# Kernel tuning notes

Measured on AMD Instinct MI355X. Metric: run time of the kernel, lower is better.

The kernel has to match this reference:

```python
import jax, jax.numpy as jnp
import numpy as np

B, S, H, D, R = 2, 2048, 16, 128, 16
HID = H * D
ROPE_BASE = 10000.0


def _rotate_half(x):
    x1, x2 = x[..., : D // 2], x[..., D // 2:]
    return jnp.concatenate((-x2, x1), axis=-1)


def _sin_cos(position_ids):
    # full-dim RoPE (rope_fraction == 1)
    inv_freq = 1.0 / (ROPE_BASE ** (jnp.arange(0, D, 2, dtype=jnp.float32) / D))  # [D/2]
    freqs = position_ids.astype(jnp.float32)[..., None] * inv_freq  # [B,S,D/2]
    emb = jnp.concatenate((freqs, freqs), axis=-1)  # [B,S,D]
    # add head axis -> [B,1,S,D]
    return jnp.sin(emb)[:, None], jnp.cos(emb)[:, None]


def setup_inputs() -> dict:
    key = jax.random.key(0)
    ks = jax.random.split(key, 6)
    q = jax.random.normal(ks[0], (B, S, HID), dtype=jnp.float32)
    k = jax.random.normal(ks[1], (B, S, HID), dtype=jnp.float32)
    v = jax.random.normal(ks[2], (B, S, HID), dtype=jnp.float32)
    position_ids = jnp.tile(jnp.arange(S, dtype=jnp.int64)[None], (B, 1))
    causal = jnp.tril(jnp.ones((S, S), dtype=bool))
    attention_mask = jnp.where(causal, 0.0, -1e9).astype(jnp.float32)
    attention_mask = jnp.broadcast_to(attention_mask[None, None], (B, 1, S, S))
    k_registers = jax.random.normal(ks[3], (1, H, R, D), dtype=jnp.float32)
    v_registers = jax.random.normal(ks[4], (1, H, R, D), dtype=jnp.float32)
    return {
        "query_states": q,
        "key_states": k,
        "value_states": v,
        "position_ids": position_ids,
        "attention_mask": attention_mask,
        "k_registers": k_registers,
        "v_registers": v_registers,
    }


def reference(query_states, key_states, value_states, position_ids,
              attention_mask, k_registers, v_registers):
    bsz, q_len, _ = query_states.shape
    # [B,S,H*D] -> [B,H,S,D]
    q = query_states.reshape(bsz, q_len, H, D).transpose(0, 2, 1, 3)
    k = key_states.reshape(bsz, -1, H, D).transpose(0, 2, 1, 3)
    v = value_states.reshape(bsz, -1, H, D).transpose(0, 2, 1, 3)

    sin, cos = _sin_cos(position_ids)
    q = q * cos + _rotate_half(q) * sin
    k = k * cos + _rotate_half(k) * sin

    # concat learned register K/V tokens along kv-length
    k = jnp.concatenate((k, jnp.broadcast_to(k_registers, (bsz, H, R, D))), axis=2)
    v = jnp.concatenate((v, jnp.broadcast_to(v_registers, (bsz, H, R, D))), axis=2)
    mask = jnp.concatenate(
        (attention_mask,
         jnp.zeros(attention_mask.shape[:-1] + (R,), dtype=attention_mask.dtype)),
        axis=-1)

    scale = 1.0 / np.sqrt(D).astype(np.float32)
    scores = jnp.einsum('bhqd,bhkd->bhqk', q, k * scale) + mask  # [B,H,S,S+R]
    probs = jax.nn.softmax(scores.astype(jnp.float32), axis=-1).astype(q.dtype)
    out = jnp.einsum('bhqk,bhkd->bhqd', probs, v)
    return out.transpose(0, 2, 1, 3).reshape(bsz, q_len, H * D)
```

## Files before the change

kernel.cpp:

```cpp
#include <hip/hip_runtime.h>

#define S_LEN 2048
#define HID   2048
#define NH    16
#define HD    128
#define NREG  16
#define KPAD  2112
#define NBH   32

typedef float f32x4 __attribute__((ext_vector_type(4)));
typedef short s16x8 __attribute__((ext_vector_type(8)));

__device__ __forceinline__ unsigned short f2bf(float f) {
    union { float f; unsigned int u; } x; x.f = f;
    return (unsigned short)((x.u + 0x7FFFu + ((x.u >> 16) & 1u)) >> 16);
}
__device__ __forceinline__ unsigned short f2bf_t(float f) {
    union { float f; unsigned int u; } x; x.f = f;
    return (unsigned short)(x.u >> 16);
}
__device__ __forceinline__ void gl_lds16(const unsigned short* g, unsigned short* l) {
    __builtin_amdgcn_global_load_lds((const __attribute__((address_space(1))) void*)g,
                                     (__attribute__((address_space(3))) void*)l, 16, 0, 0);
}

__global__ void rope_qk_kernel(const float* __restrict__ q, const float* __restrict__ k,
                               const int* __restrict__ pos,
                               unsigned short* __restrict__ Qb, unsigned short* __restrict__ Kb) {
    int i = blockIdx.x * 256 + threadIdx.x;
    int dh = i & 63;
    int h  = (i >> 6) & 15;
    int s  = (i >> 10) & 2047;
    int b  = i >> 21;
    float p   = (float)pos[b * S_LEN + s];
    float inv = exp2f((float)dh * -0.20762050593046014f);
    float ang = p * inv;
    float rev = ang * 0.15915494309189535f;
    rev -= rintf(rev);
    float a2 = rev * 6.283185307179586f;
    float sn = __sinf(a2), cs = __cosf(a2);
    const float* qp = q + (size_t)(b * S_LEN + s) * HID + h * HD + dh;
    const float* kp = k + (size_t)(b * S_LEN + s) * HID + h * HD + dh;
    float q1 = qp[0], q2 = qp[64];
    float k1 = kp[0], k2 = kp[64];
    const float scale = 0.08838834764831845f;
    size_t qo = (size_t)((b * NH + h) * S_LEN + s) * HD + dh;
    Qb[qo]      = f2bf((q1 * cs - q2 * sn) * scale);
    Qb[qo + 64] = f2bf((q2 * cs + q1 * sn) * scale);
    size_t ko = (size_t)((b * NH + h) * KPAD + s) * HD + dh;
    Kb[ko]      = f2bf(k1 * cs - k2 * sn);
    Kb[ko + 64] = f2bf(k2 * cs + k1 * sn);
}

__global__ void fill_regs_kernel(const float* __restrict__ kreg, const float* __restrict__ vreg,
                                 unsigned short* __restrict__ Kb, unsigned short* __restrict__ Vt) {
    int i = blockIdx.x * 256 + threadIdx.x;
    {
        int d = i & 127, r = (i >> 7) & 63, h = (i >> 13) & 15, b = i >> 17;
        float v = (r < NREG) ? kreg[(h * NREG + r) * HD + d] : 0.0f;
        Kb[((size_t)((b * NH + h) * KPAD + 2048 + r)) * HD + d] = f2bf(v);
    }
    {
        int r = i & 63, d = (i >> 6) & 127, h = (i >> 13) & 15, b = i >> 17;
        float v = (r < NREG) ? vreg[(h * NREG + r) * HD + d] : 0.0f;
        Vt[((size_t)((b * NH + h) * HD + d)) * KPAD + 2048 + r] = f2bf(v);
    }
}

__global__ void transpose_v_kernel(const float* __restrict__ v, unsigned short* __restrict__ Vt) {
    __shared__ unsigned short T[64][136];
    int t  = threadIdx.x;
    int bh = blockIdx.x >> 5, st = blockIdx.x & 31;
    int b  = bh >> 4, h = bh & 15;
    {
        int key = t >> 2, c = t & 3;
        const float* src = v + (size_t)(b * S_LEN + st * 64 + key) * HID + h * HD;
        #pragma unroll
        for (int i = 0; i < 4; ++i) {
            int d0 = c * 32 + i * 8;
            float4 a  = *(const float4*)(src + d0);
            float4 bb = *(const float4*)(src + d0 + 4);
            unsigned short tmp[8] = { f2bf(a.x), f2bf(a.y), f2bf(a.z), f2bf(a.w),
                                      f2bf(bb.x), f2bf(bb.y), f2bf(bb.z), f2bf(bb.w) };
            *(uint4*)(&T[key][d0]) = *(const uint4*)tmp;
        }
    }
    __syncthreads();
    {
        int d = t >> 1, half = t & 1;
        unsigned short buf[32];
        #pragma unroll
        for (int i = 0; i < 32; ++i) buf[i] = T[half * 32 + i][d];
        uint4* dst = (uint4*)(Vt + ((size_t)(bh * HD + d)) * KPAD + st * 64 + half * 32);
        const uint4* bp = (const uint4*)buf;
        #pragma unroll
        for (int i = 0; i < 4; ++i) dst[i] = bp[i];
    }
}

__global__ __launch_bounds__(256, 2)
void attn_kernel(const unsigned short* __restrict__ Qb, const unsigned short* __restrict__ Kb,
                 const unsigned short* __restrict__ Vt, float* __restrict__ out) {
    __shared__ unsigned short Klds[64 * 128];
    __shared__ unsigned short Vtl[128 * 64];
    __shared__ unsigned short Plds[4 * 32 * 72];

    int idx = blockIdx.x;
    int bh  = idx & 31;
    int j5  = idx >> 5;
    int t   = (idx < 256) ? (15 - 2 * j5) : (2 * (j5 - 8));
    int b = bh >> 4, h = bh & 15;
    int tid = threadIdx.x, w = tid >> 6, lane = tid & 63;
    int quad = lane >> 4, k15 = lane & 15;
    int s0q = t * 128;

    const unsigned short* kg[4]; unsigned short* klp[4];
    const unsigned short* vg[4]; unsigned short* vlp[4];
    {
        int krow = 16 * w + (lane >> 4);
        #pragma unroll
        for (int j = 0; j < 4; ++j) {
            int key = krow + 4 * j;
            kg[j]  = Kb + ((size_t)bh * KPAD + key) * HD + (((lane & 15) ^ (key & 15)) << 3);
            klp[j] = Klds + (16 * w + 4 * j) * HD;
        }
        int drow = 32 * w + (lane >> 3);
        int vsw  = ((lane & 7) ^ (lane >> 3)) << 3;
        #pragma unroll
        for (int j = 0; j < 4; ++j) {
            vg[j]  = Vt + ((size_t)bh * HD + drow + 8 * j) * KPAD + vsw;
            vlp[j] = Vtl + (32 * w + 8 * j) * 64;
        }
    }

    s16x8 qa[2][4];
    #pragma unroll
    for (int mt = 0; mt < 2; ++mt) {
        const unsigned short* qrow =
            Qb + ((size_t)bh * S_LEN + s0q + w * 32 + mt * 16 + k15) * HD + quad * 8;
        #pragma unroll
        for (int kc = 0; kc < 4; ++kc) qa[mt][kc] = *(const s16x8*)(qrow + kc * 32);
    }

    f32x4 oacc[2][8];
    float lsum[2][4];
    #pragma unroll
    for (int mt = 0; mt < 2; ++mt) {
        #pragma unroll
        for (int nc = 0; nc < 8; ++nc) oacc[mt][nc] = (f32x4){0.f, 0.f, 0.f, 0.f};
        #pragma unroll
        for (int r = 0; r < 4; ++r) lsum[mt][r] = 0.f;
    }

    auto stage = [&](int kbase) {
        size_t ko = (size_t)kbase * HD;
        #pragma unroll
        for (int j = 0; j < 4; ++j) gl_lds16(kg[j] + ko, klp[j]);
        #pragma unroll
        for (int j = 0; j < 4; ++j) gl_lds16(vg[j] + kbase, vlp[j]);
    };

    auto tile = [&](int coff, int mode) {
        #pragma unroll
        for (int mt = 0; mt < 2; ++mt) {
            f32x4 sc[4] = {};
            #pragma unroll
            for (int nc = 0; nc < 4; ++nc) {
                if (mode == 2 && nc > 0) continue;
                #pragma unroll
                for (int kc = 0; kc < 4; ++kc) {
                    const s16x8 bf = *(const s16x8*)(Klds + (nc * 16 + k15) * HD +
                                                     (((4 * kc + quad) ^ k15) << 3));
                    sc[nc] = __builtin_amdgcn_mfma_f32_16x16x32_bf16(qa[mt][kc], bf, sc[nc], 0, 0, 0);
                }
            }
            int rowb = w * 32 + mt * 16 + quad * 4;
            #pragma unroll
            for (int r = 0; r < 4; ++r) {
                float p[4];
                #pragma unroll
                for (int nc = 0; nc < 4; ++nc) {
                    if (mode == 2 && nc > 0) { p[nc] = 0.f; continue; }
                    float e = __expf(sc[nc][r]);
                    bool valid = (mode != 1) || (coff + nc * 16 + k15 <= rowb + r);
                    p[nc] = valid ? e : 0.f;
                }
                lsum[mt][r] += (p[0] + p[1]) + (p[2] + p[3]);
                int prow = w * (32 * 72) + (mt * 16 + quad * 4 + r) * 72 + k15;
                Plds[prow]      = f2bf_t(p[0]);
                Plds[prow + 16] = f2bf_t(p[1]);
                Plds[prow + 32] = f2bf_t(p[2]);
                Plds[prow + 48] = f2bf_t(p[3]);
            }
        }
        #pragma unroll
        for (int mt = 0; mt < 2; ++mt)
            #pragma unroll
            for (int kc = 0; kc < 2; ++kc) {
                const s16x8 pf = *(const s16x8*)(Plds + w * (32 * 72) +
                                                 (mt * 16 + k15) * 72 + kc * 32 + quad * 8);
                #pragma unroll
                for (int nc = 0; nc < 8; ++nc) {
                    const s16x8 vf = *(const s16x8*)(Vtl + (nc * 16 + k15) * 64 +
                                                     (((4 * kc + quad) ^ (k15 & 7)) << 3));
                    oacc[mt][nc] = __builtin_amdgcn_mfma_f32_16x16x32_bf16(pf, vf, oacc[mt][nc], 0, 0, 0);
                }
            }
    };

    int nfull = 2 * t;
    for (int kt = 0; kt < nfull; ++kt) {
        __syncthreads();
        stage(kt * 64);
        __syncthreads();
        tile(0, 0);
    }
    #pragma unroll
    for (int dt = 0; dt < 2; ++dt) {
        __syncthreads();
        stage((2 * t + dt) * 64);
        __syncthreads();
        tile(64 * dt, 1);
    }
    __syncthreads();
    stage(2048);
    __syncthreads();
    tile(0, 2);

    #pragma unroll
    for (int mt = 0; mt < 2; ++mt)
        #pragma unroll
        for (int r = 0; r < 4; ++r) {
            float lv = lsum[mt][r];
            #pragma unroll
            for (int off = 1; off < 16; off <<= 1) lv += __shfl_xor(lv, off);
            float invl = 1.0f / lv;
            size_t row = (size_t)(b * S_LEN + s0q + w * 32 + mt * 16 + quad * 4 + r) * HID
                         + h * HD + k15;
            #pragma unroll
            for (int nc = 0; nc < 8; ++nc)
                out[row + nc * 16] = oacc[mt][nc][r] * invl;
        }
}

extern "C" void kernel_launch(void* const* d_in, const int* in_sizes, int n_in,
                              void* d_out, int out_size, void* d_ws, size_t ws_size,
                              hipStream_t stream) {
    const float* q    = (const float*)d_in[0];
    const float* k    = (const float*)d_in[1];
    const float* v    = (const float*)d_in[2];
    const int*   pos  = (const int*)d_in[3];
    const float* kreg = (const float*)d_in[5];
    const float* vreg = (const float*)d_in[6];
    float* out = (float*)d_out;

    unsigned short* Qb = (unsigned short*)d_ws;
    unsigned short* Kb = Qb + (size_t)NBH * S_LEN * HD;
    unsigned short* Vt = Kb + (size_t)NBH * KPAD * HD;

    rope_qk_kernel<<<dim3(16384), dim3(256), 0, stream>>>(q, k, pos, Qb, Kb);
    fill_regs_kernel<<<dim3(1024), dim3(256), 0, stream>>>(kreg, vreg, Kb, Vt);
    transpose_v_kernel<<<dim3(1024), dim3(256), 0, stream>>>(v, Vt);
    attn_kernel<<<dim3(512), dim3(256), 0, stream>>>(Qb, Kb, Vt, out);
}
```

Baseline: 224.0 us.

## Merge prepass kernels and restructure attention with double-buffered V and paired tiles

The three preprocessing kernels (RoPE, register fill, V transpose) are merged into one launch, and the RoPE path is vectorized to four elements per thread. The attention kernel moves to 512 threads with 16 query rows per wave. Each block processes a pair of causal tiles (t and 15-t) so work is balanced. V is double-buffered and the next tile's loads are issued before softmax, using manual vmcnt waits, s_barrier and setprio to overlap loads with MFMA. Fewer launches and better latency hiding are traded for more complex synchronization, and the hand-written waitcnt counts could be fragile.

```diff
diff --git a/kernel.cpp b/kernel.cpp
--- a/kernel.cpp
+++ b/kernel.cpp
@@ -23,224 +23,247 @@
     __builtin_amdgcn_global_load_lds((const __attribute__((address_space(1))) void*)g,
                                      (__attribute__((address_space(3))) void*)l, 16, 0, 0);
 }
-
-__global__ void rope_qk_kernel(const float* __restrict__ q, const float* __restrict__ k,
-                               const int* __restrict__ pos,
-                               unsigned short* __restrict__ Qb, unsigned short* __restrict__ Kb) {
-    int i = blockIdx.x * 256 + threadIdx.x;
-    int dh = i & 63;
-    int h  = (i >> 6) & 15;
-    int s  = (i >> 10) & 2047;
-    int b  = i >> 21;
-    float p   = (float)pos[b * S_LEN + s];
-    float inv = exp2f((float)dh * -0.20762050593046014f);
-    float ang = p * inv;
-    float rev = ang * 0.15915494309189535f;
-    rev -= rintf(rev);
-    float a2 = rev * 6.283185307179586f;
-    float sn = __sinf(a2), cs = __cosf(a2);
-    const float* qp = q + (size_t)(b * S_LEN + s) * HID + h * HD + dh;
-    const float* kp = k + (size_t)(b * S_LEN + s) * HID + h * HD + dh;
-    float q1 = qp[0], q2 = qp[64];
-    float k1 = kp[0], k2 = kp[64];
-    const float scale = 0.08838834764831845f;
-    size_t qo = (size_t)((b * NH + h) * S_LEN + s) * HD + dh;
-    Qb[qo]      = f2bf((q1 * cs - q2 * sn) * scale);
-    Qb[qo + 64] = f2bf((q2 * cs + q1 * sn) * scale);
-    size_t ko = (size_t)((b * NH + h) * KPAD + s) * HD + dh;
-    Kb[ko]      = f2bf(k1 * cs - k2 * sn);
-    Kb[ko + 64] = f2bf(k2 * cs + k1 * sn);
-}
-
-__global__ void fill_regs_kernel(const float* __restrict__ kreg, const float* __restrict__ vreg,
-                                 unsigned short* __restrict__ Kb, unsigned short* __restrict__ Vt) {
-    int i = blockIdx.x * 256 + threadIdx.x;
-    {
-        int d = i & 127, r = (i >> 7) & 63, h = (i >> 13) & 15, b = i >> 17;
-        float v = (r < NREG) ? kreg[(h * NREG + r) * HD + d] : 0.0f;
-        Kb[((size_t)((b * NH + h) * KPAD + 2048 + r)) * HD + d] = f2bf(v);
+#define VMWAIT(n) asm volatile("s_waitcnt vmcnt(" #n ")" ::: "memory")
+__device__ __forceinline__ void bar() { asm volatile("s_barrier" ::: "memory"); }
+
+__global__ void prepass_kernel(const float* __restrict__ q, const float* __restrict__ k,
+                               const float* __restrict__ v, const int* __restrict__ pos,
+                               const float* __restrict__ kreg, const float* __restrict__ vreg,
+                               unsigned short* __restrict__ Qb, unsigned short* __restrict__ Kb,
+                               unsigned short* __restrict__ Vt) {
+    __shared__ unsigned short T[64][136];
+    int bid = blockIdx.x, tid = threadIdx.x;
+
+    if (bid < 4096) {
+        int i  = bid * 256 + tid;
+        int d4 = (i & 15) << 2;
+        int h  = (i >> 4) & 15;
+        int s  = (i >> 8) & 2047;
+        int b  = i >> 19;
+        float p = (float)pos[b * S_LEN + s];
+        const float* qp = q + (size_t)(b * S_LEN + s) * HID + h * HD + d4;
+        const float* kp = k + (size_t)(b * S_LEN + s) * HID + h * HD + d4;
+        float4 q1 = *(const float4*)qp, q2 = *(const float4*)(qp + 64);
+        float4 k1 = *(const float4*)kp, k2 = *(const float4*)(kp + 64);
+        const float* q1f = (const float*)&q1; const float* q2f = (const float*)&q2;
+        const float* k1f = (const float*)&k1; const float* k2f = (const float*)&k2;
+        const float scale = 0.08838834764831845f;
+        unsigned short oq1[4], oq2[4], ok1[4], ok2[4];
+        #pragma unroll
+        for (int j = 0; j < 4; ++j) {
+            float inv = exp2f((float)(d4 + j) * -0.20762050593046014f);
+            float rev = p * inv * 0.15915494309189535f;
+            rev -= rintf(rev);
+            float a2 = rev * 6.283185307179586f;
+            float sn = __sinf(a2), cs = __cosf(a2);
+            oq1[j] = f2bf((q1f[j] * cs - q2f[j] * sn) * scale);
+            oq2[j] = f2bf((q2f[j] * cs + q1f[j] * sn) * scale);
+            ok1[j] = f2bf(k1f[j] * cs - k2f[j] * sn);
+            ok2[j] = f2bf(k2f[j] * cs + k1f[j] * sn);
+        }
+        uint2 a;
+        size_t qo = (size_t)((b * NH + h) * S_LEN + s) * HD + d4;
+        a.x = (unsigned)oq1[0] | ((unsigned)oq1[1] << 16);
+        a.y = (unsigned)oq1[2] | ((unsigned)oq1[3] << 16);
+        *(uint2*)(Qb + qo) = a;
+        a.x = (unsigned)oq2[0] | ((unsigned)oq2[1] << 16);
+        a.y = (unsigned)oq2[2] | ((unsigned)oq2[3] << 16);
+        *(uint2*)(Qb + qo + 64) = a;
+        size_t ko = (size_t)((b * NH + h) * KPAD + s) * HD + d4;
+        a.x = (unsigned)ok1[0] | ((unsigned)ok1[1] << 16);
+        a.y = (unsigned)ok1[2] | ((unsigned)ok1[3] << 16);
+        *(uint2*)(Kb + ko) = a;
+        a.x = (unsigned)ok2[0] | ((unsigned)ok2[1] << 16);
+        a.y = (unsigned)ok2[2] | ((unsigned)ok2[3] << 16);
+        *(uint2*)(Kb + ko + 64) = a;
+    } else if (bid < 5120) {
+        int vb = bid - 4096;
+        int tt = tid;
+        int bh = vb >> 5, st = vb & 31;
+        int b  = bh >> 4, h = bh & 15;
+        {
+            int key = tt >> 2, c = tt & 3;
+            const float* src = v + (size_t)(b * S_LEN + st * 64 + key) * HID + h * HD;
+            #pragma unroll
+            for (int i = 0; i < 4; ++i) {
+                int d0 = c * 32 + i * 8;
+                float4 aa = *(const float4*)(src + d0);
+                float4 bb = *(const float4*)(src + d0 + 4);
+                unsigned short tmp[8] = { f2bf(aa.x), f2bf(aa.y), f2bf(aa.z), f2bf(aa.w),
+                                          f2bf(bb.x), f2bf(bb.y), f2bf(bb.z), f2bf(bb.w) };
+                *(uint4*)(&T[key][d0]) = *(const uint4*)tmp;
+            }
+        }
+        __syncthreads();
+        {
+            int d = tt >> 1, half = tt & 1;
+            unsigned short buf[32];
+            #pragma unroll
+            for (int i = 0; i < 32; ++i) buf[i] = T[half * 32 + i][d];
+            uint4* dst = (uint4*)(Vt + ((size_t)(bh * HD + d)) * KPAD + st * 64 + half * 32);
+            const uint4* bp = (const uint4*)buf;
+            #pragma unroll
+            for (int i = 0; i < 4; ++i) dst[i] = bp[i];
+        }
+    } else {
+        int i = (bid - 5120) * 256 + tid;
+        {
+            int d = i & 127, r = (i >> 7) & 63, h = (i >> 13) & 15, b = i >> 17;
+            float x = (r < NREG) ? kreg[(h * NREG + r) * HD + d] : 0.0f;
+            Kb[((size_t)((b * NH + h) * KPAD + 2048 + r)) * HD + d] = f2bf(x);
+        }
+        {
+            int r = i & 63, d = (i >> 6) & 127, h = (i >> 13) & 15, b = i >> 17;
+            float x = (r < NREG) ? vreg[(h * NREG + r) * HD + d] : 0.0f;
+            Vt[((size_t)((b * NH + h) * HD + d)) * KPAD + 2048 + r] = f2bf(x);
+        }
     }
-    {
-        int r = i & 63, d = (i >> 6) & 127, h = (i >> 13) & 15, b = i >> 17;
-        float v = (r < NREG) ? vreg[(h * NREG + r) * HD + d] : 0.0f;
-        Vt[((size_t)((b * NH + h) * HD + d)) * KPAD + 2048 + r] = f2bf(v);
-    }
-}
-
-__global__ void transpose_v_kernel(const float* __restrict__ v, unsigned short* __restrict__ Vt) {
-    __shared__ unsigned short T[64][136];
-    int t  = threadIdx.x;
-    int bh = blockIdx.x >> 5, st = blockIdx.x & 31;
-    int b  = bh >> 4, h = bh & 15;
-    {
-        int key = t >> 2, c = t & 3;
-        const float* src = v + (size_t)(b * S_LEN + st * 64 + key) * HID + h * HD;
-        #pragma unroll
-        for (int i = 0; i < 4; ++i) {
-            int d0 = c * 32 + i * 8;
-            float4 a  = *(const float4*)(src + d0);
-            float4 bb = *(const float4*)(src + d0 + 4);
-            unsigned short tmp[8] = { f2bf(a.x), f2bf(a.y), f2bf(a.z), f2bf(a.w),
-                                      f2bf(bb.x), f2bf(bb.y), f2bf(bb.z), f2bf(bb.w) };
-            *(uint4*)(&T[key][d0]) = *(const uint4*)tmp;
-        }
-    }
-    __syncthreads();
-    {
-        int d = t >> 1, half = t & 1;
-        unsigned short buf[32];
-        #pragma unroll
-        for (int i = 0; i < 32; ++i) buf[i] = T[half * 32 + i][d];
-        uint4* dst = (uint4*)(Vt + ((size_t)(bh * HD + d)) * KPAD + st * 64 + half * 32);
-        const uint4* bp = (const uint4*)buf;
-        #pragma unroll
-        for (int i = 0; i < 4; ++i) dst[i] = bp[i];
-    }
-}
-
-__global__ __launch_bounds__(256, 2)
+}
+
+__global__ __launch_bounds__(512, 2)
 void attn_kernel(const unsigned short* __restrict__ Qb, const unsigned short* __restrict__ Kb,
                  const unsigned short* __restrict__ Vt, float* __restrict__ out) {
     __shared__ unsigned short Klds[64 * 128];
-    __shared__ unsigned short Vtl[128 * 64];
-    __shared__ unsigned short Plds[4 * 32 * 72];
+    __shared__ unsigned short Vtl[2 * 128 * 64];
+    __shared__ unsigned short Plds[8 * 16 * 72];
 
     int idx = blockIdx.x;
     int bh  = idx & 31;
-    int j5  = idx >> 5;
-    int t   = (idx < 256) ? (15 - 2 * j5) : (2 * (j5 - 8));
+    int pr  = idx >> 5;
     int b = bh >> 4, h = bh & 15;
     int tid = threadIdx.x, w = tid >> 6, lane = tid & 63;
     int quad = lane >> 4, k15 = lane & 15;
-    int s0q = t * 128;
-
-    const unsigned short* kg[4]; unsigned short* klp[4];
-    const unsigned short* vg[4]; unsigned short* vlp[4];
-    {
-        int krow = 16 * w + (lane >> 4);
-        #pragma unroll
-        for (int j = 0; j < 4; ++j) {
-            int key = krow + 4 * j;
-            kg[j]  = Kb + ((size_t)bh * KPAD + key) * HD + (((lane & 15) ^ (key & 15)) << 3);
-            klp[j] = Klds + (16 * w + 4 * j) * HD;
-        }
-        int drow = 32 * w + (lane >> 3);
-        int vsw  = ((lane & 7) ^ (lane >> 3)) << 3;
-        #pragma unroll
-        for (int j = 0; j < 4; ++j) {
-            vg[j]  = Vt + ((size_t)bh * HD + drow + 8 * j) * KPAD + vsw;
-            vlp[j] = Vtl + (32 * w + 8 * j) * 64;
-        }
+
+    const unsigned short* kgb[2]; unsigned short* klp[2];
+    const unsigned short* vgb[2]; int vlo[2];
+    #pragma unroll
+    for (int j = 0; j < 2; ++j) {
+        int krow = 8 * w + 4 * j + (lane >> 4);
+        kgb[j] = Kb + ((size_t)bh * KPAD + krow) * HD + (((lane & 15) ^ (krow & 15)) << 3);
+        klp[j] = Klds + (8 * w + 4 * j) * HD;
+        int vrow = 16 * w + 8 * j + (lane >> 3);
+        vgb[j] = Vt + ((size_t)bh * HD + vrow) * KPAD + (((lane & 7) ^ ((lane >> 3) & 7)) << 3);
+        vlo[j] = (16 * w + 8 * j) * 64;
     }
-
-    s16x8 qa[2][4];
-    #pragma unroll
-    for (int mt = 0; mt < 2; ++mt) {
-        const unsigned short* qrow =
-            Qb + ((size_t)bh * S_LEN + s0q + w * 32 + mt * 16 + k15) * HD + quad * 8;
-        #pragma unroll
-        for (int kc = 0; kc < 4; ++kc) qa[mt][kc] = *(const s16x8*)(qrow + kc * 32);
-    }
-
-    f32x4 oacc[2][8];
-    float lsum[2][4];
-    #pragma unroll
-    for (int mt = 0; mt < 2; ++mt) {
-        #pragma unroll
-        for (int nc = 0; nc < 8; ++nc) oacc[mt][nc] = (f32x4){0.f, 0.f, 0.f, 0.f};
-        #pragma unroll
-        for (int r = 0; r < 4; ++r) lsum[mt][r] = 0.f;
-    }
-
-    auto stage = [&](int kbase) {
+    auto stageK = [&](int kbase) {
         size_t ko = (size_t)kbase * HD;
-        #pragma unroll
-        for (int j = 0; j < 4; ++j) gl_lds16(kg[j] + ko, klp[j]);
-        #pragma unroll
-        for (int j = 0; j < 4; ++j) gl_lds16(vg[j] + kbase, vlp[j]);
+        gl_lds16(kgb[0] + ko, klp[0]);
+        gl_lds16(kgb[1] + ko, klp[1]);
     };
-
-    auto tile = [&](int coff, int mode) {
-        #pragma unroll
-        for (int mt = 0; mt < 2; ++mt) {
+    auto stageV = [&](int kbase, int buf) {
+        unsigned short* vbuf = Vtl + buf * (128 * 64);
+        gl_lds16(vgb[0] + kbase, vbuf + vlo[0]);
+        gl_lds16(vgb[1] + kbase, vbuf + vlo[1]);
+    };
+
+    #pragma unroll 1
+    for (int half = 0; half < 2; ++half) {
+        int t   = half ? (15 - pr) : pr;
+        int s0q = t * 128;
+        int NT  = 2 * t + 3;
+
+        s16x8 qa[4];
+        {
+            const unsigned short* qrow =
+                Qb + ((size_t)bh * S_LEN + s0q + w * 16 + k15) * HD + quad * 8;
+            #pragma unroll
+            for (int kc = 0; kc < 4; ++kc) qa[kc] = *(const s16x8*)(qrow + kc * 32);
+        }
+        f32x4 oacc[8];
+        float lsum[4];
+        #pragma unroll
+        for (int nc = 0; nc < 8; ++nc) oacc[nc] = (f32x4){0.f, 0.f, 0.f, 0.f};
+        #pragma unroll
+        for (int r = 0; r < 4; ++r) lsum[r] = 0.f;
+
+        stageK(0);
+        stageV(0, 0);
+        VMWAIT(2);
+        bar();
+
+        int cur = 0;
+        #pragma unroll 1
+        for (int kt = 0; kt < NT; ++kt) {
+            int  mode = (kt < 2 * t) ? 0 : ((kt < 2 * t + 2) ? 1 : 2);
+            int  coff = 64 * (kt - 2 * t);
+            bool more = (kt + 1 < NT);
+            int  nkb  = (kt + 1 < 2 * t + 2) ? (kt + 1) * 64 : 2048;
+
             f32x4 sc[4] = {};
+            __builtin_amdgcn_s_setprio(1);
             #pragma unroll
             for (int nc = 0; nc < 4; ++nc) {
-                if (mode == 2 && nc > 0) continue;
-                #pragma unroll
-                for (int kc = 0; kc < 4; ++kc) {
-                    const s16x8 bf = *(const s16x8*)(Klds + (nc * 16 + k15) * HD +
-                                                     (((4 * kc + quad) ^ k15) << 3));
-                    sc[nc] = __builtin_amdgcn_mfma_f32_16x16x32_bf16(qa[mt][kc], bf, sc[nc], 0, 0, 0);
+                if (!(mode == 2 && nc > 0)) {
+                    #pragma unroll
+                    for (int kc = 0; kc < 4; ++kc) {
+                        const s16x8 bf = *(const s16x8*)(Klds + (nc * 16 + k15) * HD +
+                                                         (((4 * kc + quad) ^ k15) << 3));
+                        sc[nc] = __builtin_amdgcn_mfma_f32_16x16x32_bf16(qa[kc], bf, sc[nc], 0, 0, 0);
+                    }
                 }
             }
-            int rowb = w * 32 + mt * 16 + quad * 4;
+            __builtin_amdgcn_s_setprio(0);
+            bar();
+
+            if (more) { stageK(nkb); stageV(nkb, cur ^ 1); }
+
+            int rowb = w * 16 + quad * 4;
             #pragma unroll
             for (int r = 0; r < 4; ++r) {
-                float p[4];
+                float pv[4];
                 #pragma unroll
                 for (int nc = 0; nc < 4; ++nc) {
-                    if (mode == 2 && nc > 0) { p[nc] = 0.f; continue; }
+                    if (mode == 2 && nc > 0) { pv[nc] = 0.f; continue; }
                     float e = __expf(sc[nc][r]);
                     bool valid = (mode != 1) || (coff + nc * 16 + k15 <= rowb + r);
-                    p[nc] = valid ? e : 0.f;
+                    pv[nc] = valid ? e : 0.f;
                 }
-                lsum[mt][r] += (p[0] + p[1]) + (p[2] + p[3]);
-                int prow = w * (32 * 72) + (mt * 16 + quad * 4 + r) * 72 + k15;
-                Plds[prow]      = f2bf_t(p[0]);
-                Plds[prow + 16] = f2bf_t(p[1]);
-                Plds[prow + 32] = f2bf_t(p[2]);
-                Plds[prow + 48] = f2bf_t(p[3]);
-            }
-        }
-        #pragma unroll
-        for (int mt = 0; mt < 2; ++mt)
+                lsum[r] += (pv[0] + pv[1]) + (pv[2] + pv[3]);
+                int prow = w * 1152 + (quad * 4 + r) * 72 + k15;
+                Plds[prow]      = f2bf_t(pv[0]);
+                Plds[prow + 16] = f2bf_t(pv[1]);
+                Plds[prow + 32] = f2bf_t(pv[2]);
+                Plds[prow + 48] = f2bf_t(pv[3]);
+            }
+
+            if (more) { VMWAIT(4); } else { VMWAIT(0); }
+            bar();
+
+            const unsigned short* Vc = Vtl + cur * (128 * 64);
+            __builtin_amdgcn_s_setprio(1);
             #pragma unroll
             for (int kc = 0; kc < 2; ++kc) {
-                const s16x8 pf = *(const s16x8*)(Plds + w * (32 * 72) +
-                                                 (mt * 16 + k15) * 72 + kc * 32 + quad * 8);
-                #pragma unroll
-                for (int nc = 0; nc < 8; ++nc) {
-                    const s16x8 vf = *(const s16x8*)(Vtl + (nc * 16 + k15) * 64 +
-                                                     (((4 * kc + quad) ^ (k15 & 7)) << 3));
-                    oacc[mt][nc] = __builtin_amdgcn_mfma_f32_16x16x32_bf16(pf, vf, oacc[mt][nc], 0, 0, 0);
+                if (!(mode == 2 && kc > 0)) {
+                    const s16x8 pf = *(const s16x8*)(Plds + w * 1152 + k15 * 72 +
+                                                     kc * 32 + quad * 8);
+                    #pragma unroll
+                    for (int nc = 0; nc < 8; ++nc) {
+                        const s16x8 vf = *(const s16x8*)(Vc + (nc * 16 + k15) * 64 +
+                                                         (((4 * kc + quad) ^ (k15 & 7)) << 3));
+                        oacc[nc] = __builtin_amdgcn_mfma_f32_16x16x32_bf16(pf, vf, oacc[nc], 0, 0, 0);
+                    }
                 }
             }
-    };
-
-    int nfull = 2 * t;
-    for (int kt = 0; kt < nfull; ++kt) {
-        __syncthreads();
-        stage(kt * 64);
-        __syncthreads();
-        tile(0, 0);
-    }
-    #pragma unroll
-    for (int dt = 0; dt < 2; ++dt) {
-        __syncthreads();
-        stage((2 * t + dt) * 64);
-        __syncthreads();
-        tile(64 * dt, 1);
-    }
-    __syncthreads();
-    stage(2048);
-    __syncthreads();
-    tile(0, 2);
-
-    #pragma unroll
-    for (int mt = 0; mt < 2; ++mt)
+            __builtin_amdgcn_s_setprio(0);
+
+            if (more) { VMWAIT(2); }
+            bar();
+            cur ^= 1;
+        }
+
         #pragma unroll
         for (int r = 0; r < 4; ++r) {
-            float lv = lsum[mt][r];
+            float lv = lsum[r];
             #pragma unroll
             for (int off = 1; off < 16; off <<= 1) lv += __shfl_xor(lv, off);
             float invl = 1.0f / lv;
-            size_t row = (size_t)(b * S_LEN + s0q + w * 32 + mt * 16 + quad * 4 + r) * HID
+            size_t row = (size_t)(b * S_LEN + s0q + w * 16 + quad * 4 + r) * HID
                          + h * HD + k15;
             #pragma unroll
             for (int nc = 0; nc < 8; ++nc)
-                out[row + nc * 16] = oacc[mt][nc][r] * invl;
-        }
+                out[row + nc * 16] = oacc[nc][r] * invl;
+        }
+    }
 }
 
 extern "C" void kernel_launch(void* const* d_in, const int* in_sizes, int n_in,
@@ -258,8 +281,6 @@
     unsigned short* Kb = Qb + (size_t)NBH * S_LEN * HD;
     unsigned short* Vt = Kb + (size_t)NBH * KPAD * HD;
 
-    rope_qk_kernel<<<dim3(16384), dim3(256), 0, stream>>>(q, k, pos, Qb, Kb);
-    fill_regs_kernel<<<dim3(1024), dim3(256), 0, stream>>>(kreg, vreg, Kb, Vt);
-    transpose_v_kernel<<<dim3(1024), dim3(256), 0, stream>>>(v, Vt);
-    attn_kernel<<<dim3(512), dim3(256), 0, stream>>>(Qb, Kb, Vt, out);
-}
+    prepass_kernel<<<dim3(6144), dim3(256), 0, stream>>>(q, k, v, pos, kreg, vreg, Qb, Kb, Vt);
+    attn_kernel<<<dim3(256), dim3(512), 0, stream>>>(Qb, Kb, Vt, out);
+}
```

Measured after the change: 231.6 us. 3.4% more time.

## Merge prepass kernels into one launch and reorder MFMA loops for fragment reuse

Applied to the files above, without the earlier changes.

Folds the RoPE, V-transpose and register-fill kernels into a single prepass launch split by block index. The RoPE part now handles four elements per thread with float4 loads and packed stores. In the attention tile, the m-tile loop is moved inside so each K and V LDS fragment feeds two MFMAs, and the MFMA sections are wrapped in s_setprio. The PV stage also skips the unused kc chunk in the register-tile mode. These aim to cut launch overhead and LDS reads, but the larger live score array raises register pressure.

```diff
diff --git a/kernel.cpp b/kernel.cpp
--- a/kernel.cpp
+++ b/kernel.cpp
@@ -24,77 +24,97 @@
                                      (__attribute__((address_space(3))) void*)l, 16, 0, 0);
 }
 
-__global__ void rope_qk_kernel(const float* __restrict__ q, const float* __restrict__ k,
-                               const int* __restrict__ pos,
-                               unsigned short* __restrict__ Qb, unsigned short* __restrict__ Kb) {
-    int i = blockIdx.x * 256 + threadIdx.x;
-    int dh = i & 63;
-    int h  = (i >> 6) & 15;
-    int s  = (i >> 10) & 2047;
-    int b  = i >> 21;
-    float p   = (float)pos[b * S_LEN + s];
-    float inv = exp2f((float)dh * -0.20762050593046014f);
-    float ang = p * inv;
-    float rev = ang * 0.15915494309189535f;
-    rev -= rintf(rev);
-    float a2 = rev * 6.283185307179586f;
-    float sn = __sinf(a2), cs = __cosf(a2);
-    const float* qp = q + (size_t)(b * S_LEN + s) * HID + h * HD + dh;
-    const float* kp = k + (size_t)(b * S_LEN + s) * HID + h * HD + dh;
-    float q1 = qp[0], q2 = qp[64];
-    float k1 = kp[0], k2 = kp[64];
-    const float scale = 0.08838834764831845f;
-    size_t qo = (size_t)((b * NH + h) * S_LEN + s) * HD + dh;
-    Qb[qo]      = f2bf((q1 * cs - q2 * sn) * scale);
-    Qb[qo + 64] = f2bf((q2 * cs + q1 * sn) * scale);
-    size_t ko = (size_t)((b * NH + h) * KPAD + s) * HD + dh;
-    Kb[ko]      = f2bf(k1 * cs - k2 * sn);
-    Kb[ko + 64] = f2bf(k2 * cs + k1 * sn);
-}
-
-__global__ void fill_regs_kernel(const float* __restrict__ kreg, const float* __restrict__ vreg,
-                                 unsigned short* __restrict__ Kb, unsigned short* __restrict__ Vt) {
-    int i = blockIdx.x * 256 + threadIdx.x;
-    {
-        int d = i & 127, r = (i >> 7) & 63, h = (i >> 13) & 15, b = i >> 17;
-        float v = (r < NREG) ? kreg[(h * NREG + r) * HD + d] : 0.0f;
-        Kb[((size_t)((b * NH + h) * KPAD + 2048 + r)) * HD + d] = f2bf(v);
-    }
-    {
-        int r = i & 63, d = (i >> 6) & 127, h = (i >> 13) & 15, b = i >> 17;
-        float v = (r < NREG) ? vreg[(h * NREG + r) * HD + d] : 0.0f;
-        Vt[((size_t)((b * NH + h) * HD + d)) * KPAD + 2048 + r] = f2bf(v);
-    }
-}
-
-__global__ void transpose_v_kernel(const float* __restrict__ v, unsigned short* __restrict__ Vt) {
+__global__ void prepass_kernel(const float* __restrict__ q, const float* __restrict__ k,
+                               const float* __restrict__ v, const int* __restrict__ pos,
+                               const float* __restrict__ kreg, const float* __restrict__ vreg,
+                               unsigned short* __restrict__ Qb, unsigned short* __restrict__ Kb,
+                               unsigned short* __restrict__ Vt) {
     __shared__ unsigned short T[64][136];
-    int t  = threadIdx.x;
-    int bh = blockIdx.x >> 5, st = blockIdx.x & 31;
-    int b  = bh >> 4, h = bh & 15;
-    {
-        int key = t >> 2, c = t & 3;
-        const float* src = v + (size_t)(b * S_LEN + st * 64 + key) * HID + h * HD;
-        #pragma unroll
-        for (int i = 0; i < 4; ++i) {
-            int d0 = c * 32 + i * 8;
-            float4 a  = *(const float4*)(src + d0);
-            float4 bb = *(const float4*)(src + d0 + 4);
-            unsigned short tmp[8] = { f2bf(a.x), f2bf(a.y), f2bf(a.z), f2bf(a.w),
-                                      f2bf(bb.x), f2bf(bb.y), f2bf(bb.z), f2bf(bb.w) };
-            *(uint4*)(&T[key][d0]) = *(const uint4*)tmp;
-        }
-    }
-    __syncthreads();
-    {
-        int d = t >> 1, half = t & 1;
-        unsigned short buf[32];
-        #pragma unroll
-        for (int i = 0; i < 32; ++i) buf[i] = T[half * 32 + i][d];
-        uint4* dst = (uint4*)(Vt + ((size_t)(bh * HD + d)) * KPAD + st * 64 + half * 32);
-        const uint4* bp = (const uint4*)buf;
-        #pragma unroll
-        for (int i = 0; i < 4; ++i) dst[i] = bp[i];
+    int bid = blockIdx.x, tid = threadIdx.x;
+
+    if (bid < 4096) {
+        int i  = bid * 256 + tid;
+        int d4 = (i & 15) << 2;
+        int h  = (i >> 4) & 15;
+        int s  = (i >> 8) & 2047;
+        int b  = i >> 19;
+        float p = (float)pos[b * S_LEN + s];
+        const float* qp = q + (size_t)(b * S_LEN + s) * HID + h * HD + d4;
+        const float* kp = k + (size_t)(b * S_LEN + s) * HID + h * HD + d4;
+        float4 q1 = *(const float4*)qp, q2 = *(const float4*)(qp + 64);
+        float4 k1 = *(const float4*)kp, k2 = *(const float4*)(kp + 64);
+        const float* q1f = (const float*)&q1; const float* q2f = (const float*)&q2;
+        const float* k1f = (const float*)&k1; const float* k2f = (const float*)&k2;
+        const float scale = 0.08838834764831845f;
+        unsigned short oq1[4], oq2[4], ok1[4], ok2[4];
+        #pragma unroll
+        for (int j = 0; j < 4; ++j) {
+            float inv = exp2f((float)(d4 + j) * -0.20762050593046014f);
+            float rev = p * inv * 0.15915494309189535f;
+            rev -= rintf(rev);
+            float a2 = rev * 6.283185307179586f;
+            float sn = __sinf(a2), cs = __cosf(a2);
+            oq1[j] = f2bf((q1f[j] * cs - q2f[j] * sn) * scale);
+            oq2[j] = f2bf((q2f[j] * cs + q1f[j] * sn) * scale);
+            ok1[j] = f2bf(k1f[j] * cs - k2f[j] * sn);
+            ok2[j] = f2bf(k2f[j] * cs + k1f[j] * sn);
+        }
+        uint2 a;
+        size_t qo = (size_t)((b * NH + h) * S_LEN + s) * HD + d4;
+        a.x = (unsigned)oq1[0] | ((unsigned)oq1[1] << 16);
+        a.y = (unsigned)oq1[2] | ((unsigned)oq1[3] << 16);
+        *(uint2*)(Qb + qo) = a;
+        a.x = (unsigned)oq2[0] | ((unsigned)oq2[1] << 16);
+        a.y = (unsigned)oq2[2] | ((unsigned)oq2[3] << 16);
+        *(uint2*)(Qb + qo + 64) = a;
+        size_t ko = (size_t)((b * NH + h) * KPAD + s) * HD + d4;
+        a.x = (unsigned)ok1[0] | ((unsigned)ok1[1] << 16);
+        a.y = (unsigned)ok1[2] | ((unsigned)ok1[3] << 16);
+        *(uint2*)(Kb + ko) = a;
+        a.x = (unsigned)ok2[0] | ((unsigned)ok2[1] << 16);
+        a.y = (unsigned)ok2[2] | ((unsigned)ok2[3] << 16);
+        *(uint2*)(Kb + ko + 64) = a;
+    } else if (bid < 5120) {
+        int vb = bid - 4096;
+        int tt = tid;
+        int bh = vb >> 5, st = vb & 31;
+        int b  = bh >> 4, h = bh & 15;
+        {
+            int key = tt >> 2, c = tt & 3;
+            const float* src = v + (size_t)(b * S_LEN + st * 64 + key) * HID + h * HD;
+            #pragma unroll
+            for (int i = 0; i < 4; ++i) {
+                int d0 = c * 32 + i * 8;
+                float4 aa = *(const float4*)(src + d0);
+                float4 bb = *(const float4*)(src + d0 + 4);
+                unsigned short tmp[8] = { f2bf(aa.x), f2bf(aa.y), f2bf(aa.z), f2bf(aa.w),
+                                          f2bf(bb.x), f2bf(bb.y), f2bf(bb.z), f2bf(bb.w) };
+                *(uint4*)(&T[key][d0]) = *(const uint4*)tmp;
+            }
+        }
+        __syncthreads();
+        {
+            int d = tt >> 1, half = tt & 1;
+            unsigned short buf[32];
+            #pragma unroll
+            for (int i = 0; i < 32; ++i) buf[i] = T[half * 32 + i][d];
+            uint4* dst = (uint4*)(Vt + ((size_t)(bh * HD + d)) * KPAD + st * 64 + half * 32);
+            const uint4* bp = (const uint4*)buf;
+            #pragma unroll
+            for (int i = 0; i < 4; ++i) dst[i] = bp[i];
+        }
+    } else {
+        int i = (bid - 5120) * 256 + tid;
+        {
+            int d = i & 127, r = (i >> 7) & 63, h = (i >> 13) & 15, b = i >> 17;
+            float x = (r < NREG) ? kreg[(h * NREG + r) * HD + d] : 0.0f;
+            Kb[((size_t)((b * NH + h) * KPAD + 2048 + r)) * HD + d] = f2bf(x);
+        }
+        {
+            int r = i & 63, d = (i >> 6) & 127, h = (i >> 13) & 15, b = i >> 17;
+            float x = (r < NREG) ? vreg[(h * NREG + r) * HD + d] : 0.0f;
+            Vt[((size_t)((b * NH + h) * HD + d)) * KPAD + 2048 + r] = f2bf(x);
+        }
     }
 }
 
@@ -161,19 +181,26 @@
     };
 
     auto tile = [&](int coff, int mode) {
-        #pragma unroll
-        for (int mt = 0; mt < 2; ++mt) {
-            f32x4 sc[4] = {};
-            #pragma unroll
-            for (int nc = 0; nc < 4; ++nc) {
-                if (mode == 2 && nc > 0) continue;
+        f32x4 sc[2][4] = {};
+        __builtin_amdgcn_s_setprio(1);
+        #pragma unroll
+        for (int nc = 0; nc < 4; ++nc) {
+            if (!(mode == 2 && nc > 0)) {
                 #pragma unroll
                 for (int kc = 0; kc < 4; ++kc) {
                     const s16x8 bf = *(const s16x8*)(Klds + (nc * 16 + k15) * HD +
                                                      (((4 * kc + quad) ^ k15) << 3));
-                    sc[nc] = __builtin_amdgcn_mfma_f32_16x16x32_bf16(qa[mt][kc], bf, sc[nc], 0, 0, 0);
+                    #pragma unroll
+                    for (int mt = 0; mt < 2; ++mt)
+                        sc[mt][nc] = __builtin_amdgcn_mfma_f32_16x16x32_bf16(qa[mt][kc], bf,
+                                                                             sc[mt][nc], 0, 0, 0);
                 }
             }
+        }
+        __builtin_amdgcn_s_setprio(0);
+
+        #pragma unroll
+        for (int mt = 0; mt < 2; ++mt) {
             int rowb = w * 32 + mt * 16 + quad * 4;
             #pragma unroll
             for (int r = 0; r < 4; ++r) {
@@ -181,7 +208,7 @@
                 #pragma unroll
                 for (int nc = 0; nc < 4; ++nc) {
                     if (mode == 2 && nc > 0) { p[nc] = 0.f; continue; }
-                    float e = __expf(sc[nc][r]);
+                    float e = __expf(sc[mt][nc][r]);
                     bool valid = (mode != 1) || (coff + nc * 16 + k15 <= rowb + r);
                     p[nc] = valid ? e : 0.f;
                 }
@@ -193,19 +220,28 @@
                 Plds[prow + 48] = f2bf_t(p[3]);
             }
         }
-        #pragma unroll
-        for (int mt = 0; mt < 2; ++mt)
-            #pragma unroll
-            for (int kc = 0; kc < 2; ++kc) {
-                const s16x8 pf = *(const s16x8*)(Plds + w * (32 * 72) +
-                                                 (mt * 16 + k15) * 72 + kc * 32 + quad * 8);
+
+        __builtin_amdgcn_s_setprio(1);
+        #pragma unroll
+        for (int kc = 0; kc < 2; ++kc) {
+            if (!(mode == 2 && kc > 0)) {
+                s16x8 pf[2];
+                #pragma unroll
+                for (int mt = 0; mt < 2; ++mt)
+                    pf[mt] = *(const s16x8*)(Plds + w * (32 * 72) +
+                                             (mt * 16 + k15) * 72 + kc * 32 + quad * 8);
                 #pragma unroll
                 for (int nc = 0; nc < 8; ++nc) {
                     const s16x8 vf = *(const s16x8*)(Vtl + (nc * 16 + k15) * 64 +
                                                      (((4 * kc + quad) ^ (k15 & 7)) << 3));
-                    oacc[mt][nc] = __builtin_amdgcn_mfma_f32_16x16x32_bf16(pf, vf, oacc[mt][nc], 0, 0, 0);
+                    #pragma unroll
+                    for (int mt = 0; mt < 2; ++mt)
+                        oacc[mt][nc] = __builtin_amdgcn_mfma_f32_16x16x32_bf16(pf[mt], vf,
+                                                                               oacc[mt][nc], 0, 0, 0);
                 }
             }
+        }
+        __builtin_amdgcn_s_setprio(0);
     };
 
     int nfull = 2 * t;
@@ -258,8 +294,6 @@
     unsigned short* Kb = Qb + (size_t)NBH * S_LEN * HD;
     unsigned short* Vt = Kb + (size_t)NBH * KPAD * HD;
 
-    rope_qk_kernel<<<dim3(16384), dim3(256), 0, stream>>>(q, k, pos, Qb, Kb);
-    fill_regs_kernel<<<dim3(1024), dim3(256), 0, stream>>>(kreg, vreg, Kb, Vt);
-    transpose_v_kernel<<<dim3(1024), dim3(256), 0, stream>>>(v, Vt);
+    prepass_kernel<<<dim3(6144), dim3(256), 0, stream>>>(q, k, v, pos, kreg, vreg, Qb, Kb, Vt);
     attn_kernel<<<dim3(512), dim3(256), 0, stream>>>(Qb, Kb, Vt, out);
 }
```

After: 223.6 us. About the same (-0.2%).
